# Kernel tuning notes

Hardware: AMD Instinct MI355X
Metric: run time of the kernel (lower is better)

Reference implementation:

```python
import jax, jax.numpy as jnp
import numpy as np

NUM_CLASSES = 10
TAU = 3.3333333


def thermometer_encode(x, thresholds):
    # x: [B, F], thresholds: [F, T] -> binary bits [B, F*T]
    bits = (x[:, :, None] > thresholds[None, :, :]).astype(x.dtype)
    B = x.shape[0]
    return bits.reshape(B, -1)


def lut_layer(h, idx, luts):
    # h: [B, I] activations in [0,1]; idx: [O, n] input mapping; luts: [O, 2^n]
    # Multilinear interpolation over the 2^n LUT corners (gather + fold).
    xs = h[:, idx]                       # [B, O, n] gathered inputs
    B, O, n = xs.shape
    acc = jnp.broadcast_to(luts[None, :, :], (B, O, luts.shape[1]))  # [B, O, 2^n]
    for k in range(n):                   # fold one input bit per step (MSB first)
        half = acc.shape[-1] // 2
        xk = xs[:, :, k:k + 1]           # [B, O, 1]
        acc = acc[..., :half] * (1.0 - xk) + acc[..., half:] * xk
    return acc[..., 0]                   # [B, O]


def group_sum(h, k, tau):
    # h: [B, W] -> [B, k] popcount-style grouped sum scaled by 1/tau
    B, W = h.shape
    return h.reshape(B, k, W // k).sum(axis=-1) / tau


def setup_inputs() -> dict:
    key = jax.random.key(0)
    ks = jax.random.split(key, 6)
    B, F, T = 512, 1024, 3
    I = F * T                            # 3072 thermometer bits
    O1, O2, n = 2000, 1000, 6
    x = jax.random.normal(ks[0], (B, F), dtype=jnp.float32)
    thresholds = jax.random.normal(ks[1], (F, T), dtype=jnp.float32)
    luts1 = jax.random.uniform(ks[2], (O1, 2 ** n), dtype=jnp.float32)
    idx1 = jax.random.randint(ks[3], (O1, n), 0, I, dtype=jnp.int32)
    luts2 = jax.random.uniform(ks[4], (O2, 2 ** n), dtype=jnp.float32)
    idx2 = jax.random.randint(ks[5], (O2, n), 0, O1, dtype=jnp.int32)
    return {"x": x, "thresholds": thresholds, "luts1": luts1, "idx1": idx1,
            "luts2": luts2, "idx2": idx2}


def reference(x, thresholds, luts1, idx1, luts2, idx2):
    h = thermometer_encode(x, thresholds)     # [B, 3072] binary
    h = lut_layer(h, idx1, luts1)             # [B, 2000]
    h = lut_layer(h, idx2, luts2)             # [B, 1000]
    return group_sum(h, NUM_CLASSES, TAU)     # [B, 10]
```

## Files before the change

kernel.cpp:

```cpp
#include <hip/hip_runtime.h>


#define FEAT   1024
#define O1     2000
#define O2     1000
#define NCLS   10
#define NB     256
#define NT     1024
#define NWAVES (NB * (NT / 64))

#define WS_BITS_OFF  0
#define WS_H1_OFF    (256 << 10)
#define WS_H2_OFF    ((256 << 10) + (4 << 20))

#define SCOPE_AGENT __HIP_MEMORY_SCOPE_AGENT

__device__ unsigned g_flags[NB];

__global__ __launch_bounds__(NT, 4) void dwn_ffb(
    const float* __restrict__ x,
    const float* __restrict__ thr,
    const float* __restrict__ luts1,
    const int*   __restrict__ idx1,
    const float* __restrict__ luts2,
    const int*   __restrict__ idx2,
    float* __restrict__ out,
    unsigned long long* __restrict__ bitsT,
    float* __restrict__ h1T,
    float* __restrict__ h2T)
{
    const int t    = threadIdx.x;
    const int lane = t & 63;
    const int wl   = t >> 6;
    const int b    = blockIdx.x;
    const int gw   = (b << 4) | wl;

    const unsigned base =
        __hip_atomic_load(&g_flags[b], __ATOMIC_RELAXED, SCOPE_AGENT);

    {
        const int w8    = wl & 7;
        const int row   = (w8 << 6) | lane;
        const int fbase = (b << 2) | ((wl >> 3) << 1);
#pragma unroll
        for (int ff = 0; ff < 2; ++ff) {
            const int f = fbase + ff;
            const float xv = x[(size_t)row * FEAT + f];
            const float* tp = thr + (size_t)f * 3;
#pragma unroll
            for (int j = 0; j < 3; ++j) {
                const unsigned long long m = __ballot(xv > tp[j]);
                if (lane == 0)
                    __hip_atomic_store(&bitsT[(size_t)(f * 3 + j) * 8 + w8],
                                       m, __ATOMIC_RELAXED, SCOPE_AGENT);
            }
        }
    }

    __syncthreads();
    if (t == 0)
        __hip_atomic_store(&g_flags[b], base + 1u, __ATOMIC_RELAXED, SCOPE_AGENT);
    if (t < 64) {
        for (int spin = 0; spin < (1 << 20); ++spin) {
            const unsigned v0 = __hip_atomic_load(&g_flags[t],       __ATOMIC_RELAXED, SCOPE_AGENT);
            const unsigned v1 = __hip_atomic_load(&g_flags[t + 64],  __ATOMIC_RELAXED, SCOPE_AGENT);
            const unsigned v2 = __hip_atomic_load(&g_flags[t + 128], __ATOMIC_RELAXED, SCOPE_AGENT);
            const unsigned v3 = __hip_atomic_load(&g_flags[t + 192], __ATOMIC_RELAXED, SCOPE_AGENT);
            const unsigned tg = base + 1u;
            if (__all((v0 >= tg) & (v1 >= tg) & (v2 >= tg) & (v3 >= tg))) break;
            __builtin_amdgcn_s_sleep(2);
        }
    }
    __syncthreads();

    for (int task = gw; task < O1 * 8; task += NWAVES) {
        const int o = task >> 3;
        const int w = task & 7;
        const int* ip = idx1 + o * 6;

        const unsigned long long m0 = __hip_atomic_load(&bitsT[(size_t)ip[0] * 8 + w], __ATOMIC_RELAXED, SCOPE_AGENT);
        const unsigned long long m1 = __hip_atomic_load(&bitsT[(size_t)ip[1] * 8 + w], __ATOMIC_RELAXED, SCOPE_AGENT);
        const unsigned long long m2 = __hip_atomic_load(&bitsT[(size_t)ip[2] * 8 + w], __ATOMIC_RELAXED, SCOPE_AGENT);
        const unsigned long long m3 = __hip_atomic_load(&bitsT[(size_t)ip[3] * 8 + w], __ATOMIC_RELAXED, SCOPE_AGENT);
        const unsigned long long m4 = __hip_atomic_load(&bitsT[(size_t)ip[4] * 8 + w], __ATOMIC_RELAXED, SCOPE_AGENT);
        const unsigned long long m5 = __hip_atomic_load(&bitsT[(size_t)ip[5] * 8 + w], __ATOMIC_RELAXED, SCOPE_AGENT);

        const int code = ((int)((m0 >> lane) & 1ull) << 5)
                       | ((int)((m1 >> lane) & 1ull) << 4)
                       | ((int)((m2 >> lane) & 1ull) << 3)
                       | ((int)((m3 >> lane) & 1ull) << 2)
                       | ((int)((m4 >> lane) & 1ull) << 1)
                       |  (int)((m5 >> lane) & 1ull);

        __hip_atomic_store(&h1T[(size_t)o * 512 + (w << 6) + lane],
                           luts1[o * 64 + code], __ATOMIC_RELAXED, SCOPE_AGENT);
    }

    __syncthreads();
    if (t == 0)
        __hip_atomic_store(&g_flags[b], base + 2u, __ATOMIC_RELAXED, SCOPE_AGENT);
    if (t < 64) {
        for (int spin = 0; spin < (1 << 20); ++spin) {
            const unsigned v0 = __hip_atomic_load(&g_flags[t],       __ATOMIC_RELAXED, SCOPE_AGENT);
            const unsigned v1 = __hip_atomic_load(&g_flags[t + 64],  __ATOMIC_RELAXED, SCOPE_AGENT);
            const unsigned v2 = __hip_atomic_load(&g_flags[t + 128], __ATOMIC_RELAXED, SCOPE_AGENT);
            const unsigned v3 = __hip_atomic_load(&g_flags[t + 192], __ATOMIC_RELAXED, SCOPE_AGENT);
            const unsigned tg = base + 2u;
            if (__all((v0 >= tg) & (v1 >= tg) & (v2 >= tg) & (v3 >= tg))) break;
            __builtin_amdgcn_s_sleep(2);
        }
    }
    __syncthreads();

    for (int task = gw; task < O2 * 8; task += NWAVES) {
        const int o  = task >> 3;
        const int rr = ((task & 7) << 6) | lane;
        const int* ip = idx2 + o * 6;

        const float xv0 = __hip_atomic_load(&h1T[(size_t)ip[0] * 512 + rr], __ATOMIC_RELAXED, SCOPE_AGENT);
        const float xv1 = __hip_atomic_load(&h1T[(size_t)ip[1] * 512 + rr], __ATOMIC_RELAXED, SCOPE_AGENT);
        const float xv2 = __hip_atomic_load(&h1T[(size_t)ip[2] * 512 + rr], __ATOMIC_RELAXED, SCOPE_AGENT);
        const float xv3 = __hip_atomic_load(&h1T[(size_t)ip[3] * 512 + rr], __ATOMIC_RELAXED, SCOPE_AGENT);
        const float xv4 = __hip_atomic_load(&h1T[(size_t)ip[4] * 512 + rr], __ATOMIC_RELAXED, SCOPE_AGENT);
        const float xv5 = __hip_atomic_load(&h1T[(size_t)ip[5] * 512 + rr], __ATOMIC_RELAXED, SCOPE_AGENT);

        const float4* lp = (const float4*)(luts2 + (size_t)o * 64);
        float v[16];
#pragma unroll
        for (int q = 0; q < 16; ++q) {
            float4 e = lp[q];
            float u0 = e.x + xv5 * (e.y - e.x);
            float u1 = e.z + xv5 * (e.w - e.z);
            v[q] = u0 + xv4 * (u1 - u0);
        }
#pragma unroll
        for (int q = 0; q < 8; ++q) v[q] = v[2*q] + xv3 * (v[2*q+1] - v[2*q]);
#pragma unroll
        for (int q = 0; q < 4; ++q) v[q] = v[2*q] + xv2 * (v[2*q+1] - v[2*q]);
#pragma unroll
        for (int q = 0; q < 2; ++q) v[q] = v[2*q] + xv1 * (v[2*q+1] - v[2*q]);
        __hip_atomic_store(&h2T[(size_t)o * 512 + rr],
                           v[0] + xv0 * (v[1] - v[0]),
                           __ATOMIC_RELAXED, SCOPE_AGENT);
    }

    __syncthreads();
    if (t == 0)
        __hip_atomic_store(&g_flags[b], base + 3u, __ATOMIC_RELAXED, SCOPE_AGENT);
    if (b >= (NCLS * 8 + 15) / 16) return;
    if (t < 64) {
        for (int spin = 0; spin < (1 << 20); ++spin) {
            const unsigned v0 = __hip_atomic_load(&g_flags[t],       __ATOMIC_RELAXED, SCOPE_AGENT);
            const unsigned v1 = __hip_atomic_load(&g_flags[t + 64],  __ATOMIC_RELAXED, SCOPE_AGENT);
            const unsigned v2 = __hip_atomic_load(&g_flags[t + 128], __ATOMIC_RELAXED, SCOPE_AGENT);
            const unsigned v3 = __hip_atomic_load(&g_flags[t + 192], __ATOMIC_RELAXED, SCOPE_AGENT);
            const unsigned tg = base + 3u;
            if (__all((v0 >= tg) & (v1 >= tg) & (v2 >= tg) & (v3 >= tg))) break;
            __builtin_amdgcn_s_sleep(2);
        }
    }
    __syncthreads();

    if (gw < NCLS * 8) {
        const int c  = gw >> 3;
        const int rr = ((gw & 7) << 6) | lane;
        float s = 0.0f;
#pragma unroll
        for (int p = 0; p < 10; ++p) {
            float s2 = 0.0f;
#pragma unroll
            for (int j = 0; j < 10; ++j) {
                const float hv = __hip_atomic_load(
                    &h2T[(size_t)(c * 100 + p * 10 + j) * 512 + rr],
                    __ATOMIC_RELAXED, SCOPE_AGENT);
                s2 += hv;
            }
            s += s2;
        }
        out[(size_t)rr * NCLS + c] = s / 3.3333333f;
    }
}

extern "C" void kernel_launch(void* const* d_in, const int* in_sizes, int n_in,
                              void* d_out, int out_size, void* d_ws, size_t ws_size,
                              hipStream_t stream) {
    const float* x     = (const float*)d_in[0];
    const float* thr   = (const float*)d_in[1];
    const float* luts1 = (const float*)d_in[2];
    const int*   idx1  = (const int*)  d_in[3];
    const float* luts2 = (const float*)d_in[4];
    const int*   idx2  = (const int*)  d_in[5];
    float* out = (float*)d_out;

    char* ws = (char*)d_ws;
    unsigned long long* bitsT = (unsigned long long*)(ws + WS_BITS_OFF);
    float* h1T = (float*)(ws + WS_H1_OFF);
    float* h2T = (float*)(ws + WS_H2_OFF);

    dwn_ffb<<<NB, NT, 0, stream>>>(x, thr, luts1, idx1, luts2, idx2,
                                   out, bitsT, h1T, h2T);
}
```

Measured before the change: 97.58 us.

## Fuse layer-1 LUT lookup into layer-2, dropping h1 buffer and one grid barrier

Layer 1 is no longer materialised. Each layer-2 task recomputes its six layer-1 inputs on the fly by gathering thermometer bit masks and doing the LUT1 lookup inline. This removes the h1T global write and read traffic and one grid-wide spin barrier. In exchange, layer-1 work is recomputed about three times over (6000 recomputes against 2000 outputs per row group), adding gather loads on bitsT and idx1.

```diff
diff --git a/kernel.cpp b/kernel.cpp
--- a/kernel.cpp
+++ b/kernel.cpp
@@ -8,16 +8,16 @@
 #define NB     256
 #define NT     1024
 #define NWAVES (NB * (NT / 64))
+#define P4BLKS ((NCLS * 8 + 15) / 16)
 
 #define WS_BITS_OFF  0
-#define WS_H1_OFF    (256 << 10)
-#define WS_H2_OFF    ((256 << 10) + (4 << 20))
+#define WS_H2_OFF    (256 << 10)
 
 #define SCOPE_AGENT __HIP_MEMORY_SCOPE_AGENT
 
 __device__ unsigned g_flags[NB];
 
-__global__ __launch_bounds__(NT, 4) void dwn_ffb(
+__global__ __launch_bounds__(NT, 4) void dwn_v12(
     const float* __restrict__ x,
     const float* __restrict__ thr,
     const float* __restrict__ luts1,
@@ -26,7 +26,6 @@
     const int*   __restrict__ idx2,
     float* __restrict__ out,
     unsigned long long* __restrict__ bitsT,
-    float* __restrict__ h1T,
     float* __restrict__ h2T)
 {
     const int t    = threadIdx.x;
@@ -61,51 +60,12 @@
     if (t == 0)
         __hip_atomic_store(&g_flags[b], base + 1u, __ATOMIC_RELAXED, SCOPE_AGENT);
     if (t < 64) {
+        const unsigned tg = base + 1u;
         for (int spin = 0; spin < (1 << 20); ++spin) {
             const unsigned v0 = __hip_atomic_load(&g_flags[t],       __ATOMIC_RELAXED, SCOPE_AGENT);
             const unsigned v1 = __hip_atomic_load(&g_flags[t + 64],  __ATOMIC_RELAXED, SCOPE_AGENT);
             const unsigned v2 = __hip_atomic_load(&g_flags[t + 128], __ATOMIC_RELAXED, SCOPE_AGENT);
             const unsigned v3 = __hip_atomic_load(&g_flags[t + 192], __ATOMIC_RELAXED, SCOPE_AGENT);
-            const unsigned tg = base + 1u;
-            if (__all((v0 >= tg) & (v1 >= tg) & (v2 >= tg) & (v3 >= tg))) break;
-            __builtin_amdgcn_s_sleep(2);
-        }
-    }
-    __syncthreads();
-
-    for (int task = gw; task < O1 * 8; task += NWAVES) {
-        const int o = task >> 3;
-        const int w = task & 7;
-        const int* ip = idx1 + o * 6;
-
-        const unsigned long long m0 = __hip_atomic_load(&bitsT[(size_t)ip[0] * 8 + w], __ATOMIC_RELAXED, SCOPE_AGENT);
-        const unsigned long long m1 = __hip_atomic_load(&bitsT[(size_t)ip[1] * 8 + w], __ATOMIC_RELAXED, SCOPE_AGENT);
-        const unsigned long long m2 = __hip_atomic_load(&bitsT[(size_t)ip[2] * 8 + w], __ATOMIC_RELAXED, SCOPE_AGENT);
-        const unsigned long long m3 = __hip_atomic_load(&bitsT[(size_t)ip[3] * 8 + w], __ATOMIC_RELAXED, SCOPE_AGENT);
-        const unsigned long long m4 = __hip_atomic_load(&bitsT[(size_t)ip[4] * 8 + w], __ATOMIC_RELAXED, SCOPE_AGENT);
-        const unsigned long long m5 = __hip_atomic_load(&bitsT[(size_t)ip[5] * 8 + w], __ATOMIC_RELAXED, SCOPE_AGENT);
-
-        const int code = ((int)((m0 >> lane) & 1ull) << 5)
-                       | ((int)((m1 >> lane) & 1ull) << 4)
-                       | ((int)((m2 >> lane) & 1ull) << 3)
-                       | ((int)((m3 >> lane) & 1ull) << 2)
-                       | ((int)((m4 >> lane) & 1ull) << 1)
-                       |  (int)((m5 >> lane) & 1ull);
-
-        __hip_atomic_store(&h1T[(size_t)o * 512 + (w << 6) + lane],
-                           luts1[o * 64 + code], __ATOMIC_RELAXED, SCOPE_AGENT);
-    }
-
-    __syncthreads();
-    if (t == 0)
-        __hip_atomic_store(&g_flags[b], base + 2u, __ATOMIC_RELAXED, SCOPE_AGENT);
-    if (t < 64) {
-        for (int spin = 0; spin < (1 << 20); ++spin) {
-            const unsigned v0 = __hip_atomic_load(&g_flags[t],       __ATOMIC_RELAXED, SCOPE_AGENT);
-            const unsigned v1 = __hip_atomic_load(&g_flags[t + 64],  __ATOMIC_RELAXED, SCOPE_AGENT);
-            const unsigned v2 = __hip_atomic_load(&g_flags[t + 128], __ATOMIC_RELAXED, SCOPE_AGENT);
-            const unsigned v3 = __hip_atomic_load(&g_flags[t + 192], __ATOMIC_RELAXED, SCOPE_AGENT);
-            const unsigned tg = base + 2u;
             if (__all((v0 >= tg) & (v1 >= tg) & (v2 >= tg) & (v3 >= tg))) break;
             __builtin_amdgcn_s_sleep(2);
         }
@@ -114,47 +74,62 @@
 
     for (int task = gw; task < O2 * 8; task += NWAVES) {
         const int o  = task >> 3;
-        const int rr = ((task & 7) << 6) | lane;
+        const int w  = task & 7;
+        const int rr = (w << 6) | lane;
         const int* ip = idx2 + o * 6;
 
-        const float xv0 = __hip_atomic_load(&h1T[(size_t)ip[0] * 512 + rr], __ATOMIC_RELAXED, SCOPE_AGENT);
-        const float xv1 = __hip_atomic_load(&h1T[(size_t)ip[1] * 512 + rr], __ATOMIC_RELAXED, SCOPE_AGENT);
-        const float xv2 = __hip_atomic_load(&h1T[(size_t)ip[2] * 512 + rr], __ATOMIC_RELAXED, SCOPE_AGENT);
-        const float xv3 = __hip_atomic_load(&h1T[(size_t)ip[3] * 512 + rr], __ATOMIC_RELAXED, SCOPE_AGENT);
-        const float xv4 = __hip_atomic_load(&h1T[(size_t)ip[4] * 512 + rr], __ATOMIC_RELAXED, SCOPE_AGENT);
-        const float xv5 = __hip_atomic_load(&h1T[(size_t)ip[5] * 512 + rr], __ATOMIC_RELAXED, SCOPE_AGENT);
+        float xv[6];
+#pragma unroll
+        for (int k = 0; k < 6; ++k) {
+            const int o1 = ip[k];
+            const int2* iq = (const int2*)(idx1 + o1 * 6);
+            const int2 q0 = iq[0], q1 = iq[1], q2 = iq[2];
+            const unsigned long long m0 = __hip_atomic_load(&bitsT[(size_t)q0.x * 8 + w], __ATOMIC_RELAXED, SCOPE_AGENT);
+            const unsigned long long m1 = __hip_atomic_load(&bitsT[(size_t)q0.y * 8 + w], __ATOMIC_RELAXED, SCOPE_AGENT);
+            const unsigned long long m2 = __hip_atomic_load(&bitsT[(size_t)q1.x * 8 + w], __ATOMIC_RELAXED, SCOPE_AGENT);
+            const unsigned long long m3 = __hip_atomic_load(&bitsT[(size_t)q1.y * 8 + w], __ATOMIC_RELAXED, SCOPE_AGENT);
+            const unsigned long long m4 = __hip_atomic_load(&bitsT[(size_t)q2.x * 8 + w], __ATOMIC_RELAXED, SCOPE_AGENT);
+            const unsigned long long m5 = __hip_atomic_load(&bitsT[(size_t)q2.y * 8 + w], __ATOMIC_RELAXED, SCOPE_AGENT);
+            const int code = ((int)((m0 >> lane) & 1ull) << 5)
+                           | ((int)((m1 >> lane) & 1ull) << 4)
+                           | ((int)((m2 >> lane) & 1ull) << 3)
+                           | ((int)((m3 >> lane) & 1ull) << 2)
+                           | ((int)((m4 >> lane) & 1ull) << 1)
+                           |  (int)((m5 >> lane) & 1ull);
+            xv[k] = luts1[o1 * 64 + code];
+        }
 
         const float4* lp = (const float4*)(luts2 + (size_t)o * 64);
         float v[16];
 #pragma unroll
         for (int q = 0; q < 16; ++q) {
             float4 e = lp[q];
-            float u0 = e.x + xv5 * (e.y - e.x);
-            float u1 = e.z + xv5 * (e.w - e.z);
-            v[q] = u0 + xv4 * (u1 - u0);
+            float u0 = e.x + xv[5] * (e.y - e.x);
+            float u1 = e.z + xv[5] * (e.w - e.z);
+            v[q] = u0 + xv[4] * (u1 - u0);
         }
 #pragma unroll
-        for (int q = 0; q < 8; ++q) v[q] = v[2*q] + xv3 * (v[2*q+1] - v[2*q]);
+        for (int q = 0; q < 8; ++q) v[q] = v[2*q] + xv[3] * (v[2*q+1] - v[2*q]);
 #pragma unroll
-        for (int q = 0; q < 4; ++q) v[q] = v[2*q] + xv2 * (v[2*q+1] - v[2*q]);
+        for (int q = 0; q < 4; ++q) v[q] = v[2*q] + xv[2] * (v[2*q+1] - v[2*q]);
 #pragma unroll
-        for (int q = 0; q < 2; ++q) v[q] = v[2*q] + xv1 * (v[2*q+1] - v[2*q]);
+        for (int q = 0; q < 2; ++q) v[q] = v[2*q] + xv[1] * (v[2*q+1] - v[2*q]);
         __hip_atomic_store(&h2T[(size_t)o * 512 + rr],
-                           v[0] + xv0 * (v[1] - v[0]),
+                           v[0] + xv[0] * (v[1] - v[0]),
                            __ATOMIC_RELAXED, SCOPE_AGENT);
     }
 
     __syncthreads();
     if (t == 0)
-        __hip_atomic_store(&g_flags[b], base + 3u, __ATOMIC_RELAXED, SCOPE_AGENT);
-    if (b >= (NCLS * 8 + 15) / 16) return;
+        __hip_atomic_store(&g_flags[b], base + 2u, __ATOMIC_RELAXED, SCOPE_AGENT);
+    if (b >= P4BLKS) return;
     if (t < 64) {
+        const unsigned tg = base + 2u;
         for (int spin = 0; spin < (1 << 20); ++spin) {
             const unsigned v0 = __hip_atomic_load(&g_flags[t],       __ATOMIC_RELAXED, SCOPE_AGENT);
             const unsigned v1 = __hip_atomic_load(&g_flags[t + 64],  __ATOMIC_RELAXED, SCOPE_AGENT);
             const unsigned v2 = __hip_atomic_load(&g_flags[t + 128], __ATOMIC_RELAXED, SCOPE_AGENT);
             const unsigned v3 = __hip_atomic_load(&g_flags[t + 192], __ATOMIC_RELAXED, SCOPE_AGENT);
-            const unsigned tg = base + 3u;
             if (__all((v0 >= tg) & (v1 >= tg) & (v2 >= tg) & (v3 >= tg))) break;
             __builtin_amdgcn_s_sleep(2);
         }
@@ -194,9 +169,8 @@
 
     char* ws = (char*)d_ws;
     unsigned long long* bitsT = (unsigned long long*)(ws + WS_BITS_OFF);
-    float* h1T = (float*)(ws + WS_H1_OFF);
     float* h2T = (float*)(ws + WS_H2_OFF);
 
-    dwn_ffb<<<NB, NT, 0, stream>>>(x, thr, luts1, idx1, luts2, idx2,
-                                   out, bitsT, h1T, h2T);
+    dwn_v12<<<NB, NT, 0, stream>>>(x, thr, luts1, idx1, luts2, idx2,
+                                   out, bitsT, h2T);
 }
```

Measured after the change: 98.88 us. No clear change (+1.3%).
